# Kernel optimization log

Measured on AMD Instinct MI355X. Metric: run time of the kernel, lower is better.

Reference implementation:

```python
import jax, jax.numpy as jnp
import numpy as np

D_MODEL = 1024
H = 16
D_K = D_MODEL // H
B, S = 2, 2048

def setup_inputs() -> dict:
    key = jax.random.key(0)
    ks = jax.random.split(key, 13)
    scale = 1.0 / np.sqrt(D_MODEL)
    mk = lambda k: jax.random.normal(k, (D_MODEL, D_MODEL), dtype=jnp.float32) * scale
    return {
        'q': jax.random.normal(ks[0], (B, S, D_MODEL), dtype=jnp.float32),
        'k': jax.random.normal(ks[1], (B, S, D_MODEL), dtype=jnp.float32),
        'v': jax.random.normal(ks[2], (B, S, D_MODEL), dtype=jnp.float32),
        'mask': jax.random.randint(ks[3], (B, 1, S, S), 0, 2, dtype=jnp.int32),
        'wq': mk(ks[4]), 'bq': jnp.zeros((D_MODEL,), jnp.float32),
        'wk': mk(ks[5]), 'bk': jnp.zeros((D_MODEL,), jnp.float32),
        'wv': mk(ks[6]), 'bv': jnp.zeros((D_MODEL,), jnp.float32),
        'wo': mk(ks[7]), 'bo': jnp.zeros((D_MODEL,), jnp.float32),
    }

def reference(q, k, v, mask, wq, bq, wk, bk, wv, bv, wo, bo):
    b, s, _ = q.shape
    # linear projections then split heads: [B,S,D] -> [B,H,S,Dk]
    def proj(x, w, bias):
        y = x @ w + bias
        return y.reshape(b, -1, H, D_K).transpose(0, 2, 1, 3)
    Q = proj(q, wq, bq)
    K = proj(k, wk, bk)
    V = proj(v, wv, bv)
    scores = jnp.einsum('bhqd,bhkd->bhqk', Q, K) / jnp.sqrt(jnp.float32(D_K))
    # faithful to source: masked positions are set to 1e-9 (not -inf)
    scores = jnp.where(mask == 0, jnp.float32(1e-9), scores)
    attn = jax.nn.softmax(scores, axis=-1)  # dropout is identity in eval mode
    x = jnp.einsum('bhqk,bhkd->bhqd', attn, V)
    x = x.transpose(0, 2, 1, 3).reshape(b, s, D_MODEL)
    return x @ wo + bo
```

## Files before the change

### kernel.cpp

```cpp
#include <hip/hip_runtime.h>
#include <hip/hip_bf16.h>

#define DM 1024
#define HEADS 16
#define DKK 64
#define BB 2
#define SS 2048
#define MROWS (BB*SS)

typedef __attribute__((ext_vector_type(8))) short bf16x8;
typedef __attribute__((ext_vector_type(4))) float f32x4;
typedef __hip_bfloat16 bf16;

#define SC2 0.1803368801f
#define MB2 1.442695041e-9f

__device__ __forceinline__ void async16(const void* g, void* l) {
    __builtin_amdgcn_global_load_lds((const __attribute__((address_space(1))) void*)g,
                                     (__attribute__((address_space(3))) void*)l, 16, 0, 0);
}

__global__ void prep_kernel(const float* __restrict__ q, const float* __restrict__ k,
                            const float* __restrict__ v,
                            const float* __restrict__ wq, const float* __restrict__ wk,
                            const float* __restrict__ wv, const float* __restrict__ wo,
                            const int* __restrict__ mask,
                            bf16* __restrict__ qkv, bf16* __restrict__ wcat,
                            unsigned long long* __restrict__ bits) {
    __shared__ float tile[32][33];
    const int bid = blockIdx.x;
    const int tid = threadIdx.x;
    if (bid < 12288) {
        const int z = bid >> 12;
        const int i = ((bid & 4095) << 8) + tid;
        const float* src = z == 0 ? q : (z == 1 ? k : v);
        float4 val = ((const float4*)src)[i];
        union { bf16 b[4]; ushort4 u; } cvt;
        cvt.b[0] = __float2bfloat16(val.x);
        cvt.b[1] = __float2bfloat16(val.y);
        cvt.b[2] = __float2bfloat16(val.z);
        cvt.b[3] = __float2bfloat16(val.w);
        ((ushort4*)(qkv + (size_t)z * MROWS * DM))[i] = cvt.u;
    } else if (bid < 12288 + 4096) {
        const int t = bid - 12288;
        const int z = t >> 10;
        const int bx = t & 31, by = (t >> 5) & 31;
        const float* src = z == 0 ? wq : (z == 1 ? wk : (z == 2 ? wv : wo));
        bf16* dst = wcat + ((size_t)z << 20);
        const int tx = tid & 31, ty = tid >> 5;
        const int x = bx * 32 + tx, y0 = by * 32 + ty;
#pragma unroll
        for (int i = 0; i < 32; i += 8)
            tile[ty + i][tx] = src[(size_t)(y0 + i) * DM + x];
        __syncthreads();
        const int nx = by * 32 + tx, ny0 = bx * 32 + ty;
#pragma unroll
        for (int i = 0; i < 32; i += 8)
            dst[(size_t)(ny0 + i) * DM + nx] = __float2bfloat16(tile[tx][ty + i]);
    } else {
        const int i = ((bid - 16384) << 8) + tid;
        unsigned long long b = __ballot(mask[i] != 0);
        if ((tid & 63) == 0) bits[i >> 6] = b;
    }
}

__global__ __launch_bounds__(256) void gemm_qkv(const bf16* __restrict__ qb, const bf16* __restrict__ kb,
                                                const bf16* __restrict__ vb, const bf16* __restrict__ wcat,
                                                const float* __restrict__ bq, const float* __restrict__ bk,
                                                const float* __restrict__ bv,
                                                bf16* __restrict__ Qh, bf16* __restrict__ Kh,
                                                bf16* __restrict__ Vt) {
    __shared__ __align__(16) bf16 lA[128 * 32];
    __shared__ __align__(16) bf16 lB[128 * 32];
    const int seg = blockIdx.x >> 3;
    const bf16* A    = seg == 0 ? qb : (seg == 1 ? kb : vb);
    const bf16* Bt   = wcat + ((size_t)seg << 20);
    const float* bias = seg == 0 ? bq : (seg == 1 ? bk : bv);

    const int tid  = threadIdx.x;
    const int lane = tid & 63;
    const int lm   = lane & 15;
    const int quad = lane >> 4;
    const int w    = tid >> 6;
    const int wm   = w >> 1, wn = w & 1;
    const int m0   = blockIdx.y * 128;
    const int n0   = (blockIdx.x & 7) * 128;
    const int wbase = w << 6;

    f32x4 acc[4][4];
#pragma unroll
    for (int i = 0; i < 4; ++i)
#pragma unroll
        for (int j = 0; j < 4; ++j) acc[i][j] = (f32x4){0.f, 0.f, 0.f, 0.f};

    for (int kt = 0; kt < DM / 32; ++kt) {
#pragma unroll
        for (int r = 0; r < 2; ++r) {
            const int idx = r * 256 + tid;
            const int row = idx >> 2;
            const int kc  = idx & 3;
            async16(A + (size_t)(m0 + row) * DM + kt * 32 + kc * 8,
                    (char*)lA + (size_t)(r * 256 + wbase) * 16);
            async16(Bt + (size_t)(n0 + row) * DM + kt * 32 + kc * 8,
                    (char*)lB + (size_t)(r * 256 + wbase) * 16);
        }
        __syncthreads();
        bf16x8 af[4], bb[4];
#pragma unroll
        for (int mt = 0; mt < 4; ++mt)
            af[mt] = *(const bf16x8*)&lA[(wm * 64 + mt * 16 + lm) * 32 + quad * 8];
#pragma unroll
        for (int nt = 0; nt < 4; ++nt)
            bb[nt] = *(const bf16x8*)&lB[(wn * 64 + nt * 16 + lm) * 32 + quad * 8];
#pragma unroll
        for (int mt = 0; mt < 4; ++mt)
#pragma unroll
            for (int nt = 0; nt < 4; ++nt)
                acc[mt][nt] = __builtin_amdgcn_mfma_f32_16x16x32_bf16(af[mt], bb[nt], acc[mt][nt], 0, 0, 0);
        __syncthreads();
    }

    bf16* outQK = seg == 0 ? Qh : Kh;
    const float oscale = (seg == 1) ? SC2 : 1.0f;
#pragma unroll
    for (int mt = 0; mt < 4; ++mt) {
#pragma unroll
        for (int nt = 0; nt < 4; ++nt) {
            const int gcol = n0 + wn * 64 + nt * 16 + lm;
            const float bvv = bias[gcol];
            const int h = gcol >> 6, d = gcol & 63;
#pragma unroll
            for (int r = 0; r < 4; ++r) {
                const int grow = m0 + wm * 64 + mt * 16 + quad * 4 + r;
                const int b = grow >> 11, s = grow & 2047;
                const float val = (acc[mt][nt][r] + bvv) * oscale;
                if (seg < 2)
                    outQK[((size_t)(b * HEADS + h) * SS + s) * DKK + d] = __float2bfloat16(val);
                else
                    Vt[((size_t)(b * HEADS + h) * DKK + d) * SS + s] = __float2bfloat16(val);
            }
        }
    }
}

__global__ __launch_bounds__(256) void gemm_out(const bf16* __restrict__ A, const bf16* __restrict__ Bt,
                                                const float* __restrict__ bias, float* __restrict__ outp) {
    __shared__ __align__(16) bf16 lA[128 * 32];
    __shared__ __align__(16) bf16 lB[64 * 32];
    const int tid  = threadIdx.x;
    const int lane = tid & 63;
    const int lm   = lane & 15;
    const int quad = lane >> 4;
    const int w    = tid >> 6;
    const int m0   = blockIdx.y * 128;
    const int n0   = blockIdx.x * 64;
    const int wbase = w << 6;

    f32x4 acc[2][4];
#pragma unroll
    for (int i = 0; i < 2; ++i)
#pragma unroll
        for (int j = 0; j < 4; ++j) acc[i][j] = (f32x4){0.f, 0.f, 0.f, 0.f};

    for (int kt = 0; kt < DM / 32; ++kt) {
#pragma unroll
        for (int r = 0; r < 2; ++r) {
            const int idx = r * 256 + tid;
            const int row = idx >> 2;
            const int kc  = idx & 3;
            async16(A + (size_t)(m0 + row) * DM + kt * 32 + kc * 8,
                    (char*)lA + (size_t)(r * 256 + wbase) * 16);
        }
        {
            const int row = tid >> 2;
            const int kc  = tid & 3;
            async16(Bt + (size_t)(n0 + row) * DM + kt * 32 + kc * 8,
                    (char*)lB + (size_t)(wbase) * 16);
        }
        __syncthreads();
        bf16x8 af[2], bb[4];
#pragma unroll
        for (int mt = 0; mt < 2; ++mt)
            af[mt] = *(const bf16x8*)&lA[(w * 32 + mt * 16 + lm) * 32 + quad * 8];
#pragma unroll
        for (int nt = 0; nt < 4; ++nt)
            bb[nt] = *(const bf16x8*)&lB[(nt * 16 + lm) * 32 + quad * 8];
#pragma unroll
        for (int mt = 0; mt < 2; ++mt)
#pragma unroll
            for (int nt = 0; nt < 4; ++nt)
                acc[mt][nt] = __builtin_amdgcn_mfma_f32_16x16x32_bf16(af[mt], bb[nt], acc[mt][nt], 0, 0, 0);
        __syncthreads();
    }

#pragma unroll
    for (int mt = 0; mt < 2; ++mt)
#pragma unroll
        for (int nt = 0; nt < 4; ++nt) {
            const int gcol = n0 + nt * 16 + lm;
            const float bvv = bias[gcol];
#pragma unroll
            for (int r = 0; r < 4; ++r) {
                const int grow = m0 + w * 32 + mt * 16 + quad * 4 + r;
                outp[(size_t)grow * DM + gcol] = acc[mt][nt][r] + bvv;
            }
        }
}

__global__ __launch_bounds__(256, 4) void attn_kernel(const bf16* __restrict__ Qh, const bf16* __restrict__ Kh,
                                                      const bf16* __restrict__ Vt,
                                                      const unsigned long long* __restrict__ mbits,
                                                      bf16* __restrict__ ctx) {
    __shared__ __align__(16) bf16 ldsK[2][64 * 64];
    __shared__ __align__(16) bf16 ldsV[2][64 * 64];
    __shared__ __align__(16) bf16 ldsP[4][16 * 64];

    const int tid  = threadIdx.x;
    const int lane = tid & 63;
    const int lm   = lane & 15;
    const int quad = lane >> 4;
    const int w    = tid >> 6;
    const int bh   = blockIdx.y;
    const int b    = bh >> 4;
    const int h    = bh & 15;
    const int q0   = blockIdx.x * 64;
    const int qrow = q0 + w * 16 + lm;

    const int x0 = quad ^ (lm & 7);
    const int x1 = x0 ^ 4;

    const int L0 = tid, L1 = 256 + tid;
    const int row0 = L0 >> 3, sw0 = (L0 & 7) ^ (row0 & 7);
    const int row1 = L1 >> 3, sw1 = (L1 & 7) ^ (row1 & 7);
    const bf16* kbase = Kh + (size_t)bh * SS * DKK;
    const bf16* vbase = Vt + (size_t)bh * DKK * SS;
    const bf16* pK0 = kbase + (size_t)row0 * DKK + sw0 * 8;
    const bf16* pK1 = kbase + (size_t)row1 * DKK + sw1 * 8;
    const bf16* pV0 = vbase + (size_t)row0 * SS + sw0 * 8;
    const bf16* pV1 = vbase + (size_t)row1 * SS + sw1 * 8;
    char* dKa[2] = { (char*)ldsK[0] + (size_t)(w * 64) * 16, (char*)ldsK[1] + (size_t)(w * 64) * 16 };
    char* dKb[2] = { (char*)ldsK[0] + (size_t)(256 + w * 64) * 16, (char*)ldsK[1] + (size_t)(256 + w * 64) * 16 };
    char* dVa[2] = { (char*)ldsV[0] + (size_t)(w * 64) * 16, (char*)ldsV[1] + (size_t)(w * 64) * 16 };
    char* dVb[2] = { (char*)ldsV[0] + (size_t)(256 + w * 64) * 16, (char*)ldsV[1] + (size_t)(256 + w * 64) * 16 };

    const bf16* qp = Qh + ((size_t)bh * SS + qrow) * DKK;
    const bf16x8 aq0 = *(const bf16x8*)(qp + quad * 8);
    const bf16x8 aq1 = *(const bf16x8*)(qp + 32 + quad * 8);

    const unsigned long long* pm = mbits + ((size_t)b * SS + qrow) * (SS / 64);

    f32x4 o[4];
#pragma unroll
    for (int i = 0; i < 4; ++i) o[i] = (f32x4){0.f, 0.f, 0.f, 0.f};
    float lsum = 0.f;
    bf16* pmy = &ldsP[w][0];

    async16(pK0, dKa[0]);
    async16(pK1, dKb[0]);
    async16(pV0, dVa[0]);
    async16(pV1, dVb[0]);
    __syncthreads();

    const int nkt = SS / 64;

    auto body = [&](int it, int cur) {
        const unsigned long long mw = pm[it];
        if (it + 1 < nkt) {
            const int nb = cur ^ 1;
            const size_t ko = (size_t)(it + 1) * 64;
            async16(pK0 + ko * DKK, dKa[nb]);
            async16(pK1 + ko * DKK, dKb[nb]);
            async16(pV0 + ko, dVa[nb]);
            async16(pV1 + ko, dVb[nb]);
        }
        const bf16* lk = ldsK[cur];
        const bf16* lv = ldsV[cur];

        f32x4 sc[4];
#pragma unroll
        for (int mt = 0; mt < 4; ++mt) {
            sc[mt] = (f32x4){0.f, 0.f, 0.f, 0.f};
            const bf16x8 kf0 = *(const bf16x8*)&lk[(mt * 16 + lm) * 64 + x0 * 8];
            const bf16x8 kf1 = *(const bf16x8*)&lk[(mt * 16 + lm) * 64 + x1 * 8];
            sc[mt] = __builtin_amdgcn_mfma_f32_16x16x32_bf16(kf0, aq0, sc[mt], 0, 0, 0);
            sc[mt] = __builtin_amdgcn_mfma_f32_16x16x32_bf16(kf1, aq1, sc[mt], 0, 0, 0);
        }

        const unsigned long long mq = mw >> (quad * 4);
#pragma unroll
        for (int mt = 0; mt < 4; ++mt) {
            const unsigned int mmt = (unsigned int)(mq >> (mt * 16));
            union { bf16 hh[4]; uint2 u; } pk;
#pragma unroll
            for (int r = 0; r < 4; ++r) {
                const float sv = ((mmt >> r) & 1u) ? sc[mt][r] : MB2;
                const float p = __builtin_amdgcn_exp2f(sv);
                lsum += p;
                pk.hh[r] = __float2bfloat16(p);
            }
            *(uint2*)&pmy[lm * 64 + (((mt * 2 + (quad >> 1)) ^ (lm & 7)) << 3) + ((quad & 1) << 2)] = pk.u;
        }

        const bf16x8 pf0 = *(const bf16x8*)&pmy[lm * 64 + x0 * 8];
        const bf16x8 pf1 = *(const bf16x8*)&pmy[lm * 64 + x1 * 8];
#pragma unroll
        for (int mt = 0; mt < 4; ++mt) {
            const bf16x8 vf0 = *(const bf16x8*)&lv[(mt * 16 + lm) * 64 + x0 * 8];
            const bf16x8 vf1 = *(const bf16x8*)&lv[(mt * 16 + lm) * 64 + x1 * 8];
            o[mt] = __builtin_amdgcn_mfma_f32_16x16x32_bf16(vf0, pf0, o[mt], 0, 0, 0);
            o[mt] = __builtin_amdgcn_mfma_f32_16x16x32_bf16(vf1, pf1, o[mt], 0, 0, 0);
        }

        __syncthreads();
    };

    for (int it = 0; it < nkt; it += 2) {
        body(it, 0);
        body(it + 1, 1);
    }

    lsum += __shfl_xor(lsum, 16);
    lsum += __shfl_xor(lsum, 32);
    const float rl = 1.0f / lsum;

    bf16* crow = ctx + ((size_t)b * SS + qrow) * DM + h * DKK;
#pragma unroll
    for (int mt = 0; mt < 4; ++mt) {
        union { bf16 hh[4]; uint2 u; } pk;
#pragma unroll
        for (int r = 0; r < 4; ++r) pk.hh[r] = __float2bfloat16(o[mt][r] * rl);
        *(uint2*)&crow[mt * 16 + quad * 4] = pk.u;
    }
}

extern "C" void kernel_launch(void* const* d_in, const int* in_sizes, int n_in,
                              void* d_out, int out_size, void* d_ws, size_t ws_size,
                              hipStream_t stream) {
    const float* q  = (const float*)d_in[0];
    const float* k  = (const float*)d_in[1];
    const float* v  = (const float*)d_in[2];
    const int* mask = (const int*)d_in[3];
    const float* wq = (const float*)d_in[4];
    const float* bq = (const float*)d_in[5];
    const float* wk = (const float*)d_in[6];
    const float* bk = (const float*)d_in[7];
    const float* wv = (const float*)d_in[8];
    const float* bv = (const float*)d_in[9];
    const float* wo = (const float*)d_in[10];
    const float* bo = (const float*)d_in[11];

    const size_t MB = 1ull << 20;
    char* ws = (char*)d_ws;
    bf16* qkv  = (bf16*)(ws + 0 * MB);
    bf16* wcat = (bf16*)(ws + 24 * MB);
    bf16* wot  = (bf16*)(ws + 30 * MB);
    bf16* Qh   = (bf16*)(ws + 32 * MB);
    bf16* Kh   = (bf16*)(ws + 40 * MB);
    bf16* Vt   = (bf16*)(ws + 48 * MB);
    bf16* ctx  = (bf16*)(ws + 56 * MB);
    unsigned long long* mbits = (unsigned long long*)(ws + 64 * MB);

    prep_kernel<<<49152, 256, 0, stream>>>(q, k, v, wq, wk, wv, wo, mask, qkv, wcat, mbits);

    gemm_qkv<<<dim3(24, 32), 256, 0, stream>>>(qkv, qkv + (size_t)MROWS * DM, qkv + 2 * (size_t)MROWS * DM,
                                               wcat, bq, bk, bv, Qh, Kh, Vt);

    attn_kernel<<<dim3(SS / 64, BB * HEADS), 256, 0, stream>>>(Qh, Kh, Vt, mbits, ctx);

    gemm_out<<<dim3(DM / 64, MROWS / 128), 256, 0, stream>>>(ctx, wot, bo, (float*)d_out);
}
```

Measured before the change: 271.8 us.

## Split attention key tiles across two wave groups, use permlane swaps for P

After: 282.8 us. +4.0%, slower.

```diff
diff --git a/kernel.cpp b/kernel.cpp
--- a/kernel.cpp
+++ b/kernel.cpp
@@ -10,6 +10,7 @@
 
 typedef __attribute__((ext_vector_type(8))) short bf16x8;
 typedef __attribute__((ext_vector_type(4))) float f32x4;
+typedef __attribute__((ext_vector_type(2))) unsigned int uv2;
 typedef __hip_bfloat16 bf16;
 
 #define SC2 0.1803368801f
@@ -58,9 +59,17 @@
         for (int i = 0; i < 32; i += 8)
             dst[(size_t)(ny0 + i) * DM + nx] = __float2bfloat16(tile[tx][ty + i]);
     } else {
-        const int i = ((bid - 16384) << 8) + tid;
-        unsigned long long b = __ballot(mask[i] != 0);
-        if ((tid & 63) == 0) bits[i >> 6] = b;
+        const int i4 = ((bid - 16384) << 8) + tid;
+        const int4 m = ((const int4*)mask)[i4];
+        unsigned long long vv = (unsigned long long)(
+            (m.x != 0 ? 1u : 0u) | (m.y != 0 ? 2u : 0u) |
+            (m.z != 0 ? 4u : 0u) | (m.w != 0 ? 8u : 0u));
+        vv <<= ((tid & 15) * 4);
+        vv |= __shfl_xor(vv, 1);
+        vv |= __shfl_xor(vv, 2);
+        vv |= __shfl_xor(vv, 4);
+        vv |= __shfl_xor(vv, 8);
+        if ((tid & 15) == 0) bits[i4 >> 4] = vv;
     }
 }
 
@@ -120,24 +129,39 @@
         __syncthreads();
     }
 
-    bf16* outQK = seg == 0 ? Qh : Kh;
-    const float oscale = (seg == 1) ? SC2 : 1.0f;
-#pragma unroll
-    for (int mt = 0; mt < 4; ++mt) {
-#pragma unroll
-        for (int nt = 0; nt < 4; ++nt) {
-            const int gcol = n0 + wn * 64 + nt * 16 + lm;
-            const float bvv = bias[gcol];
-            const int h = gcol >> 6, d = gcol & 63;
-#pragma unroll
-            for (int r = 0; r < 4; ++r) {
-                const int grow = m0 + wm * 64 + mt * 16 + quad * 4 + r;
-                const int b = grow >> 11, s = grow & 2047;
-                const float val = (acc[mt][nt][r] + bvv) * oscale;
-                if (seg < 2)
+    if (seg < 2) {
+        bf16* outQK = seg == 0 ? Qh : Kh;
+        const float oscale = (seg == 1) ? SC2 : 1.0f;
+#pragma unroll
+        for (int mt = 0; mt < 4; ++mt) {
+#pragma unroll
+            for (int nt = 0; nt < 4; ++nt) {
+                const int gcol = n0 + wn * 64 + nt * 16 + lm;
+                const float bvv = bias[gcol];
+                const int h = gcol >> 6, d = gcol & 63;
+#pragma unroll
+                for (int r = 0; r < 4; ++r) {
+                    const int grow = m0 + wm * 64 + mt * 16 + quad * 4 + r;
+                    const int b = grow >> 11, s = grow & 2047;
+                    const float val = (acc[mt][nt][r] + bvv) * oscale;
                     outQK[((size_t)(b * HEADS + h) * SS + s) * DKK + d] = __float2bfloat16(val);
-                else
-                    Vt[((size_t)(b * HEADS + h) * DKK + d) * SS + s] = __float2bfloat16(val);
+                }
+            }
+        }
+    } else {
+#pragma unroll
+        for (int mt = 0; mt < 4; ++mt) {
+#pragma unroll
+            for (int nt = 0; nt < 4; ++nt) {
+                const int gcol = n0 + wn * 64 + nt * 16 + lm;
+                const float bvv = bias[gcol];
+                const int h = gcol >> 6, d = gcol & 63;
+                const int growb = m0 + wm * 64 + mt * 16 + quad * 4;
+                const int b = growb >> 11, s = growb & 2047;
+                union { bf16 hh[4]; uint2 u; } pk;
+#pragma unroll
+                for (int r = 0; r < 4; ++r) pk.hh[r] = __float2bfloat16(acc[mt][nt][r] + bvv);
+                *(uint2*)&Vt[((size_t)(b * HEADS + h) * DKK + d) * SS + s] = pk.u;
             }
         }
     }
@@ -207,41 +231,36 @@
         }
 }
 
-__global__ __launch_bounds__(256, 4) void attn_kernel(const bf16* __restrict__ Qh, const bf16* __restrict__ Kh,
+__global__ __launch_bounds__(512, 8) void attn_kernel(const bf16* __restrict__ Qh, const bf16* __restrict__ Kh,
                                                       const bf16* __restrict__ Vt,
                                                       const unsigned long long* __restrict__ mbits,
                                                       bf16* __restrict__ ctx) {
     __shared__ __align__(16) bf16 ldsK[2][64 * 64];
     __shared__ __align__(16) bf16 ldsV[2][64 * 64];
-    __shared__ __align__(16) bf16 ldsP[4][16 * 64];
 
     const int tid  = threadIdx.x;
     const int lane = tid & 63;
     const int lm   = lane & 15;
     const int quad = lane >> 4;
     const int w    = tid >> 6;
+    const int wq   = w & 3;
+    const int kh   = w >> 2;
     const int bh   = blockIdx.y;
     const int b    = bh >> 4;
     const int h    = bh & 15;
     const int q0   = blockIdx.x * 64;
-    const int qrow = q0 + w * 16 + lm;
+    const int qrow = q0 + wq * 16 + lm;
 
     const int x0 = quad ^ (lm & 7);
     const int x1 = x0 ^ 4;
-
-    const int L0 = tid, L1 = 256 + tid;
-    const int row0 = L0 >> 3, sw0 = (L0 & 7) ^ (row0 & 7);
-    const int row1 = L1 >> 3, sw1 = (L1 & 7) ^ (row1 & 7);
-    const bf16* kbase = Kh + (size_t)bh * SS * DKK;
-    const bf16* vbase = Vt + (size_t)bh * DKK * SS;
-    const bf16* pK0 = kbase + (size_t)row0 * DKK + sw0 * 8;
-    const bf16* pK1 = kbase + (size_t)row1 * DKK + sw1 * 8;
-    const bf16* pV0 = vbase + (size_t)row0 * SS + sw0 * 8;
-    const bf16* pV1 = vbase + (size_t)row1 * SS + sw1 * 8;
-    char* dKa[2] = { (char*)ldsK[0] + (size_t)(w * 64) * 16, (char*)ldsK[1] + (size_t)(w * 64) * 16 };
-    char* dKb[2] = { (char*)ldsK[0] + (size_t)(256 + w * 64) * 16, (char*)ldsK[1] + (size_t)(256 + w * 64) * 16 };
-    char* dVa[2] = { (char*)ldsV[0] + (size_t)(w * 64) * 16, (char*)ldsV[1] + (size_t)(w * 64) * 16 };
-    char* dVb[2] = { (char*)ldsV[0] + (size_t)(256 + w * 64) * 16, (char*)ldsV[1] + (size_t)(256 + w * 64) * 16 };
+    const int xh = kh ? x1 : x0;
+
+    const int srow = tid >> 3;
+    const int sw   = (tid & 7) ^ (srow & 7);
+    const bf16* pK = Kh + (size_t)bh * SS * DKK + (size_t)srow * DKK + sw * 8;
+    const bf16* pV = Vt + (size_t)bh * DKK * SS + (size_t)srow * SS + sw * 8;
+    char* dK[2] = { (char*)ldsK[0] + (size_t)(w * 64) * 16, (char*)ldsK[1] + (size_t)(w * 64) * 16 };
+    char* dV[2] = { (char*)ldsV[0] + (size_t)(w * 64) * 16, (char*)ldsV[1] + (size_t)(w * 64) * 16 };
 
     const bf16* qp = Qh + ((size_t)bh * SS + qrow) * DKK;
     const bf16x8 aq0 = *(const bf16x8*)(qp + quad * 8);
@@ -253,64 +272,67 @@
 #pragma unroll
     for (int i = 0; i < 4; ++i) o[i] = (f32x4){0.f, 0.f, 0.f, 0.f};
     float lsum = 0.f;
-    bf16* pmy = &ldsP[w][0];
-
-    async16(pK0, dKa[0]);
-    async16(pK1, dKb[0]);
-    async16(pV0, dVa[0]);
-    async16(pV1, dVb[0]);
+
+    async16(pK, dK[0]);
+    async16(pV, dV[0]);
     __syncthreads();
 
     const int nkt = SS / 64;
+    const int mshift = kh * 32 + quad * 4;
 
     auto body = [&](int it, int cur) {
         const unsigned long long mw = pm[it];
         if (it + 1 < nkt) {
             const int nb = cur ^ 1;
-            const size_t ko = (size_t)(it + 1) * 64;
-            async16(pK0 + ko * DKK, dKa[nb]);
-            async16(pK1 + ko * DKK, dKb[nb]);
-            async16(pV0 + ko, dVa[nb]);
-            async16(pV1 + ko, dVb[nb]);
+            async16(pK + (size_t)(it + 1) * 64 * DKK, dK[nb]);
+            async16(pV + (size_t)(it + 1) * 64, dV[nb]);
         }
         const bf16* lk = ldsK[cur];
         const bf16* lv = ldsV[cur];
 
-        f32x4 sc[4];
-#pragma unroll
-        for (int mt = 0; mt < 4; ++mt) {
-            sc[mt] = (f32x4){0.f, 0.f, 0.f, 0.f};
+        f32x4 sc[2];
+#pragma unroll
+        for (int mtl = 0; mtl < 2; ++mtl) {
+            const int mt = kh * 2 + mtl;
+            sc[mtl] = (f32x4){0.f, 0.f, 0.f, 0.f};
             const bf16x8 kf0 = *(const bf16x8*)&lk[(mt * 16 + lm) * 64 + x0 * 8];
             const bf16x8 kf1 = *(const bf16x8*)&lk[(mt * 16 + lm) * 64 + x1 * 8];
-            sc[mt] = __builtin_amdgcn_mfma_f32_16x16x32_bf16(kf0, aq0, sc[mt], 0, 0, 0);
-            sc[mt] = __builtin_amdgcn_mfma_f32_16x16x32_bf16(kf1, aq1, sc[mt], 0, 0, 0);
-        }
-
-        const unsigned long long mq = mw >> (quad * 4);
+            sc[mtl] = __builtin_amdgcn_mfma_f32_16x16x32_bf16(kf0, aq0, sc[mtl], 0, 0, 0);
+            sc[mtl] = __builtin_amdgcn_mfma_f32_16x16x32_bf16(kf1, aq1, sc[mtl], 0, 0, 0);
+        }
+
+        const unsigned long long mq = mw >> mshift;
+        unsigned wds[4];
+#pragma unroll
+        for (int mtl = 0; mtl < 2; ++mtl) {
+            const unsigned mmt = (unsigned)(mq >> (mtl * 16));
+#pragma unroll
+            for (int pp = 0; pp < 2; ++pp) {
+                union { bf16 hh[2]; unsigned u; } wu;
+#pragma unroll
+                for (int j = 0; j < 2; ++j) {
+                    const int r = pp * 2 + j;
+                    const float sv = ((mmt >> r) & 1u) ? sc[mtl][r] : MB2;
+                    const float p = __builtin_amdgcn_exp2f(sv);
+                    lsum += p;
+                    wu.hh[j] = __float2bfloat16(p);
+                }
+                wds[mtl * 2 + pp] = wu.u;
+            }
+        }
+
+        const uv2 s1 = __builtin_amdgcn_permlane32_swap(wds[0], wds[2], false, false);
+        const uv2 s2 = __builtin_amdgcn_permlane16_swap(s1.x, s1.y, false, false);
+        const uv2 s3 = __builtin_amdgcn_permlane32_swap(wds[1], wds[3], false, false);
+        const uv2 s4 = __builtin_amdgcn_permlane16_swap(s3.x, s3.y, false, false);
+        union { unsigned u[4]; bf16x8 v; } pf;
+        pf.u[0] = s2.x; pf.u[1] = s4.x; pf.u[2] = s2.y; pf.u[3] = s4.y;
+
 #pragma unroll
         for (int mt = 0; mt < 4; ++mt) {
-            const unsigned int mmt = (unsigned int)(mq >> (mt * 16));
-            union { bf16 hh[4]; uint2 u; } pk;
-#pragma unroll
-            for (int r = 0; r < 4; ++r) {
-                const float sv = ((mmt >> r) & 1u) ? sc[mt][r] : MB2;
-                const float p = __builtin_amdgcn_exp2f(sv);
-                lsum += p;
-                pk.hh[r] = __float2bfloat16(p);
-            }
-            *(uint2*)&pmy[lm * 64 + (((mt * 2 + (quad >> 1)) ^ (lm & 7)) << 3) + ((quad & 1) << 2)] = pk.u;
-        }
-
-        const bf16x8 pf0 = *(const bf16x8*)&pmy[lm * 64 + x0 * 8];
-        const bf16x8 pf1 = *(const bf16x8*)&pmy[lm * 64 + x1 * 8];
-#pragma unroll
-        for (int mt = 0; mt < 4; ++mt) {
-            const bf16x8 vf0 = *(const bf16x8*)&lv[(mt * 16 + lm) * 64 + x0 * 8];
-            const bf16x8 vf1 = *(const bf16x8*)&lv[(mt * 16 + lm) * 64 + x1 * 8];
-            o[mt] = __builtin_amdgcn_mfma_f32_16x16x32_bf16(vf0, pf0, o[mt], 0, 0, 0);
-            o[mt] = __builtin_amdgcn_mfma_f32_16x16x32_bf16(vf1, pf1, o[mt], 0, 0, 0);
-        }
-
+            const bf16x8 vf = *(const bf16x8*)&lv[(mt * 16 + lm) * 64 + xh * 8];
+            o[mt] = __builtin_amdgcn_mfma_f32_16x16x32_bf16(vf, pf.v, o[mt], 0, 0, 0);
+        }
         __syncthreads();
     };
 
@@ -321,15 +343,31 @@
 
     lsum += __shfl_xor(lsum, 16);
     lsum += __shfl_xor(lsum, 32);
-    const float rl = 1.0f / lsum;
-
-    bf16* crow = ctx + ((size_t)b * SS + qrow) * DM + h * DKK;
-#pragma unroll
-    for (int mt = 0; mt < 4; ++mt) {
-        union { bf16 hh[4]; uint2 u; } pk;
-#pragma unroll
-        for (int r = 0; r < 4; ++r) pk.hh[r] = __float2bfloat16(o[mt][r] * rl);
-        *(uint2*)&crow[mt * 16 + quad * 4] = pk.u;
+
+    float* oshare = (float*)ldsK;
+    float* lshare = (float*)ldsV;
+    if (kh == 1) {
+#pragma unroll
+        for (int mt = 0; mt < 4; ++mt)
+            *(f32x4*)&oshare[(size_t)(wq * 16 + lm) * 64 + mt * 16 + quad * 4] = o[mt];
+        if (lane < 16) lshare[wq * 16 + lane] = lsum;
+    }
+    __syncthreads();
+    if (kh == 0) {
+#pragma unroll
+        for (int mt = 0; mt < 4; ++mt)
+            o[mt] += *(const f32x4*)&oshare[(size_t)(wq * 16 + lm) * 64 + mt * 16 + quad * 4];
+        lsum += lshare[wq * 16 + lm];
+        const float rl = 1.0f / lsum;
+
+        bf16* crow = ctx + ((size_t)b * SS + qrow) * DM + h * DKK;
+#pragma unroll
+        for (int mt = 0; mt < 4; ++mt) {
+            union { bf16 hh[4]; uint2 u; } pk;
+#pragma unroll
+            for (int r = 0; r < 4; ++r) pk.hh[r] = __float2bfloat16(o[mt][r] * rl);
+            *(uint2*)&crow[mt * 16 + quad * 4] = pk.u;
+        }
     }
 }
 
@@ -360,12 +398,12 @@
     bf16* ctx  = (bf16*)(ws + 56 * MB);
     unsigned long long* mbits = (unsigned long long*)(ws + 64 * MB);
 
-    prep_kernel<<<49152, 256, 0, stream>>>(q, k, v, wq, wk, wv, wo, mask, qkv, wcat, mbits);
+    prep_kernel<<<24576, 256, 0, stream>>>(q, k, v, wq, wk, wv, wo, mask, qkv, wcat, mbits);
 
     gemm_qkv<<<dim3(24, 32), 256, 0, stream>>>(qkv, qkv + (size_t)MROWS * DM, qkv + 2 * (size_t)MROWS * DM,
                                                wcat, bq, bk, bv, Qh, Kh, Vt);
 
-    attn_kernel<<<dim3(SS / 64, BB * HEADS), 256, 0, stream>>>(Qh, Kh, Vt, mbits, ctx);
+    attn_kernel<<<dim3(SS / 64, BB * HEADS), 512, 0, stream>>>(Qh, Kh, Vt, mbits, ctx);
 
     gemm_out<<<dim3(DM / 64, MROWS / 128), 256, 0, stream>>>(ctx, wot, bo, (float*)d_out);
 }
```

## Vectorize mask packing, swap GEMM grid order, pack V-transpose stores

Applied to the files above, without the earlier changes.

After: 266.1 us. 2.1% less time.

```diff
diff --git a/kernel.cpp b/kernel.cpp
--- a/kernel.cpp
+++ b/kernel.cpp
@@ -58,9 +58,17 @@
         for (int i = 0; i < 32; i += 8)
             dst[(size_t)(ny0 + i) * DM + nx] = __float2bfloat16(tile[tx][ty + i]);
     } else {
-        const int i = ((bid - 16384) << 8) + tid;
-        unsigned long long b = __ballot(mask[i] != 0);
-        if ((tid & 63) == 0) bits[i >> 6] = b;
+        const int i4 = ((bid - 16384) << 8) + tid;
+        const int4 m = ((const int4*)mask)[i4];
+        unsigned long long vv = (unsigned long long)(
+            (m.x != 0 ? 1u : 0u) | (m.y != 0 ? 2u : 0u) |
+            (m.z != 0 ? 4u : 0u) | (m.w != 0 ? 8u : 0u));
+        vv <<= ((tid & 15) * 4);
+        vv |= __shfl_xor(vv, 1);
+        vv |= __shfl_xor(vv, 2);
+        vv |= __shfl_xor(vv, 4);
+        vv |= __shfl_xor(vv, 8);
+        if ((tid & 15) == 0) bits[i4 >> 4] = vv;
     }
 }
 
@@ -72,7 +80,7 @@
                                                 bf16* __restrict__ Vt) {
     __shared__ __align__(16) bf16 lA[128 * 32];
     __shared__ __align__(16) bf16 lB[128 * 32];
-    const int seg = blockIdx.x >> 3;
+    const int seg = blockIdx.y >> 3;
     const bf16* A    = seg == 0 ? qb : (seg == 1 ? kb : vb);
     const bf16* Bt   = wcat + ((size_t)seg << 20);
     const float* bias = seg == 0 ? bq : (seg == 1 ? bk : bv);
@@ -83,8 +91,8 @@
     const int quad = lane >> 4;
     const int w    = tid >> 6;
     const int wm   = w >> 1, wn = w & 1;
-    const int m0   = blockIdx.y * 128;
-    const int n0   = (blockIdx.x & 7) * 128;
+    const int m0   = blockIdx.x * 128;
+    const int n0   = (blockIdx.y & 7) * 128;
     const int wbase = w << 6;
 
     f32x4 acc[4][4];
@@ -120,24 +128,39 @@
         __syncthreads();
     }
 
-    bf16* outQK = seg == 0 ? Qh : Kh;
-    const float oscale = (seg == 1) ? SC2 : 1.0f;
-#pragma unroll
-    for (int mt = 0; mt < 4; ++mt) {
-#pragma unroll
-        for (int nt = 0; nt < 4; ++nt) {
-            const int gcol = n0 + wn * 64 + nt * 16 + lm;
-            const float bvv = bias[gcol];
-            const int h = gcol >> 6, d = gcol & 63;
-#pragma unroll
-            for (int r = 0; r < 4; ++r) {
-                const int grow = m0 + wm * 64 + mt * 16 + quad * 4 + r;
-                const int b = grow >> 11, s = grow & 2047;
-                const float val = (acc[mt][nt][r] + bvv) * oscale;
-                if (seg < 2)
+    if (seg < 2) {
+        bf16* outQK = seg == 0 ? Qh : Kh;
+        const float oscale = (seg == 1) ? SC2 : 1.0f;
+#pragma unroll
+        for (int mt = 0; mt < 4; ++mt) {
+#pragma unroll
+            for (int nt = 0; nt < 4; ++nt) {
+                const int gcol = n0 + wn * 64 + nt * 16 + lm;
+                const float bvv = bias[gcol];
+                const int h = gcol >> 6, d = gcol & 63;
+#pragma unroll
+                for (int r = 0; r < 4; ++r) {
+                    const int grow = m0 + wm * 64 + mt * 16 + quad * 4 + r;
+                    const int b = grow >> 11, s = grow & 2047;
+                    const float val = (acc[mt][nt][r] + bvv) * oscale;
                     outQK[((size_t)(b * HEADS + h) * SS + s) * DKK + d] = __float2bfloat16(val);
-                else
-                    Vt[((size_t)(b * HEADS + h) * DKK + d) * SS + s] = __float2bfloat16(val);
+                }
+            }
+        }
+    } else {
+#pragma unroll
+        for (int mt = 0; mt < 4; ++mt) {
+#pragma unroll
+            for (int nt = 0; nt < 4; ++nt) {
+                const int gcol = n0 + wn * 64 + nt * 16 + lm;
+                const float bvv = bias[gcol];
+                const int h = gcol >> 6, d = gcol & 63;
+                const int growb = m0 + wm * 64 + mt * 16 + quad * 4;
+                const int b = growb >> 11, s = growb & 2047;
+                union { bf16 hh[4]; uint2 u; } pk;
+#pragma unroll
+                for (int r = 0; r < 4; ++r) pk.hh[r] = __float2bfloat16(acc[mt][nt][r] + bvv);
+                *(uint2*)&Vt[((size_t)(b * HEADS + h) * DKK + d) * SS + s] = pk.u;
             }
         }
     }
@@ -152,8 +175,8 @@
     const int lm   = lane & 15;
     const int quad = lane >> 4;
     const int w    = tid >> 6;
-    const int m0   = blockIdx.y * 128;
-    const int n0   = blockIdx.x * 64;
+    const int m0   = blockIdx.x * 128;
+    const int n0   = blockIdx.y * 64;
     const int wbase = w << 6;
 
     f32x4 acc[2][4];
@@ -360,12 +383,12 @@
     bf16* ctx  = (bf16*)(ws + 56 * MB);
     unsigned long long* mbits = (unsigned long long*)(ws + 64 * MB);
 
-    prep_kernel<<<49152, 256, 0, stream>>>(q, k, v, wq, wk, wv, wo, mask, qkv, wcat, mbits);
-
-    gemm_qkv<<<dim3(24, 32), 256, 0, stream>>>(qkv, qkv + (size_t)MROWS * DM, qkv + 2 * (size_t)MROWS * DM,
+    prep_kernel<<<24576, 256, 0, stream>>>(q, k, v, wq, wk, wv, wo, mask, qkv, wcat, mbits);
+
+    gemm_qkv<<<dim3(32, 24), 256, 0, stream>>>(qkv, qkv + (size_t)MROWS * DM, qkv + 2 * (size_t)MROWS * DM,
                                                wcat, bq, bk, bv, Qh, Kh, Vt);
 
     attn_kernel<<<dim3(SS / 64, BB * HEADS), 256, 0, stream>>>(Qh, Kh, Vt, mbits, ctx);
 
-    gemm_out<<<dim3(DM / 64, MROWS / 128), 256, 0, stream>>>(ctx, wot, bo, (float*)d_out);
-}
+    gemm_out<<<dim3(32, DM / 64), 256, 0, stream>>>(ctx, wot, bo, (float*)d_out);
+}
```
